# Kernel tuning notes

Hardware: AMD Instinct MI355X
Metric: run time of the kernel (lower is better)

## Reference

```python
import jax, jax.numpy as jnp
import numpy as np

EPS_RMS = 1.1920929e-07  # torch.finfo(float32).eps (nn.RMSNorm default eps=None)
EPS_LN = 1e-5
SCALE = 64 ** -0.5       # Attention.scale uses default dim_head=64, NOT dim_head_qk
SOFTCLAMP = 5.0
DEPTH = 4
H, DQK, DV = 8, 128, 192
D, DP = 768, 128
SEQ, NPAIR, B = 2048, 256, 1
FF_INNER = int(D * 2.0)
DP_INNER = int(DP * 2.0)
MAX_POS = 8192


def rmsnorm(x, w):
    return x * jax.lax.rsqrt(jnp.mean(x * x, axis=-1, keepdims=True) + EPS_RMS) * w


def layernorm_nb(x, w):  # LayerNorm(bias=False)
    mu = jnp.mean(x, axis=-1, keepdims=True)
    var = jnp.mean((x - mu) ** 2, axis=-1, keepdims=True)
    return (x - mu) * jax.lax.rsqrt(var + EPS_LN) * w


def rotate_half(x):
    x1, x2 = jnp.split(x, 2, axis=-1)
    return jnp.concatenate((-x2, x1), axis=-1)


def apply_rotary(pos, t):
    return t * jnp.cos(pos) + rotate_half(t) * jnp.sin(pos)


def rotary_table(seq_len):
    # faithful to source: inv_freq = 1/(arange(nf) + logspace(1, max_pos-nf+1, nf))
    nf = DQK // 2
    inv_freq = 1.0 / (jnp.arange(nf, dtype=jnp.float32)
                      + 10.0 ** jnp.linspace(1.0, float(MAX_POS - nf + 1), nf, dtype=jnp.float32))
    freqs = jnp.arange(seq_len, dtype=jnp.float32)[:, None] * inv_freq  # [n, nf]
    return jnp.concatenate((freqs, freqs), axis=-1)  # [n, DQK]


def softclamp(t):
    return jnp.tanh(t / SOFTCLAMP) * SOFTCLAMP


def _forward(single, pairwise, attn_pre_w, attn_post_w, qkv_w, q_norm_w, k_norm_w,
             v_norm_w, bias_rms_w, bias_proj_w, out_w, ff_pre_w, ff_post_w,
             ff_w1, ff_b1, ff_w2, ff_b2, pw_attn_pre_w, pw_qk_w, pw_v_w, pw_v_b,
             pw_ff_pre_w, pw_ff_w1, pw_ff_b1, pw_ff_w2, pw_ff_b2):
    b, n, _ = single.shape
    pos = rotary_table(n)
    pw_idx = 0
    for i in range(DEPTH):
        # ---- attention block (sandwich RMSNorm) ----
        res = single
        xn = rmsnorm(single, attn_pre_w[i])
        qkv = xn @ qkv_w[i]
        q, k, v = jnp.split(qkv, [H * DQK, H * DQK + DQK], axis=-1)
        q = q.reshape(b, n, H, DQK).transpose(0, 2, 1, 3)  # b h n d (k,v are single-head)
        q = layernorm_nb(q, q_norm_w[i]) * SCALE
        k = layernorm_nb(k, k_norm_w[i])
        v = layernorm_nb(v, v_norm_w[i])
        q = apply_rotary(pos, q)
        k = apply_rotary(pos, k)
        sim = jnp.einsum('bhid,bjd->bhij', q, k)
        # pairwise bias: RMSNorm -> GELU -> Linear(dp, heads) -> b h i j, nearest-repeat to seq
        pb = jax.nn.gelu(rmsnorm(pairwise, bias_rms_w[i]), approximate=False) @ bias_proj_w[i]
        pb = pb.transpose(0, 3, 1, 2)  # b h i j
        r = sim.shape[-1] // pb.shape[-1]
        pb = jnp.repeat(jnp.repeat(pb, r, axis=2), r, axis=3)
        attn = jax.nn.softmax(softclamp(sim + pb), axis=-1)
        out = jnp.einsum('bhij,bjd->bhid', attn, v)
        out = out.transpose(0, 2, 1, 3).reshape(b, n, H * DV)
        single = rmsnorm(out @ out_w[i], attn_post_w[i]) + res
        # ---- feedforward (sandwich RMSNorm) ----
        res = single
        xn = rmsnorm(single, ff_pre_w[i])
        h = jax.nn.relu(xn @ ff_w1[i] + ff_b1[i])
        single = rmsnorm(h @ ff_w2[i] + ff_b2[i], ff_post_w[i]) + res
        # ---- pairwise track every other layer (no sandwich) ----
        if i % 2 == 0:
            j = pw_idx
            res = pairwise
            xn = rmsnorm(pairwise, pw_attn_pre_w[j])
            pq, pk = jnp.split(xn @ pw_qk_w[j], 2, axis=-1)
            pv = xn @ pw_v_w[j] + pw_v_b[j]
            psim = jnp.einsum('bnid,bnjd->bnij', pq, pk)  # source never applies its scale
            pairwise = jnp.einsum('bnij,bnjd->bnid', jax.nn.softmax(psim, axis=-1), pv) + res
            res = pairwise
            xn = rmsnorm(pairwise, pw_ff_pre_w[j])
            hh = jax.nn.relu(xn @ pw_ff_w1[j] + pw_ff_b1[j])
            pairwise = hh @ pw_ff_w2[j] + pw_ff_b2[j] + res
            pw_idx += 1
    return single, pairwise


def setup_inputs() -> dict:
    key = jax.random.key(0)
    ks = iter(jax.random.split(key, 40))
    nrm = lambda shape: jax.random.normal(next(ks), shape, jnp.float32) * 0.02
    n_pw = (DEPTH + 1) // 2
    return dict(
        single=jax.random.normal(next(ks), (B, SEQ, D), jnp.float32),
        pairwise=jax.random.normal(next(ks), (B, NPAIR, NPAIR, DP), jnp.float32),
        attn_pre_w=jnp.ones((DEPTH, D), jnp.float32),
        attn_post_w=jnp.ones((DEPTH, D), jnp.float32),
        qkv_w=nrm((DEPTH, D, H * DQK + DQK + DV)),
        q_norm_w=jnp.ones((DEPTH, DQK), jnp.float32),
        k_norm_w=jnp.ones((DEPTH, DQK), jnp.float32),
        v_norm_w=jnp.ones((DEPTH, DV), jnp.float32),
        bias_rms_w=jnp.ones((DEPTH, DP), jnp.float32),
        bias_proj_w=nrm((DEPTH, DP, H)),
        out_w=nrm((DEPTH, H * DV, D)),
        ff_pre_w=jnp.ones((DEPTH, D), jnp.float32),
        ff_post_w=jnp.ones((DEPTH, D), jnp.float32),
        ff_w1=nrm((DEPTH, D, FF_INNER)),
        ff_b1=jnp.zeros((DEPTH, FF_INNER), jnp.float32),
        ff_w2=nrm((DEPTH, FF_INNER, D)),
        ff_b2=jnp.zeros((DEPTH, D), jnp.float32),
        pw_attn_pre_w=jnp.ones((n_pw, DP), jnp.float32),
        pw_qk_w=nrm((n_pw, DP, 2 * DP)),
        pw_v_w=nrm((n_pw, DP, DP)),
        pw_v_b=jnp.zeros((n_pw, DP), jnp.float32),
        pw_ff_pre_w=jnp.ones((n_pw, DP), jnp.float32),
        pw_ff_w1=nrm((n_pw, DP, DP_INNER)),
        pw_ff_b1=jnp.zeros((n_pw, DP_INNER), jnp.float32),
        pw_ff_w2=nrm((n_pw, DP_INNER, DP)),
        pw_ff_b2=jnp.zeros((n_pw, DP), jnp.float32),
    )


def reference(single, pairwise, attn_pre_w, attn_post_w, qkv_w, q_norm_w, k_norm_w,
              v_norm_w, bias_rms_w, bias_proj_w, out_w, ff_pre_w, ff_post_w,
              ff_w1, ff_b1, ff_w2, ff_b2, pw_attn_pre_w, pw_qk_w, pw_v_w, pw_v_b,
              pw_ff_pre_w, pw_ff_w1, pw_ff_b1, pw_ff_w2, pw_ff_b2):
    return _forward(single, pairwise, attn_pre_w, attn_post_w, qkv_w, q_norm_w,
                    k_norm_w, v_norm_w, bias_rms_w, bias_proj_w, out_w, ff_pre_w,
                    ff_post_w, ff_w1, ff_b1, ff_w2, ff_b2, pw_attn_pre_w, pw_qk_w,
                    pw_v_w, pw_v_b, pw_ff_pre_w, pw_ff_w1, pw_ff_b1, pw_ff_w2, pw_ff_b2)
```

## Files before the change

### kernel.cpp

```cpp
#include <hip/hip_runtime.h>
#include <hip/hip_bf16.h>

#define SEQ 2048
#define DMODEL 768
#define NHEAD 8
#define DQK 128
#define DV 192
#define QKVN 1344
#define FFI 1536
#define NP 256
#define DP 128
#define DPI 256
#define NPR 65536
#define KVB 64
#define NSPLIT 2

#define EPS_RMS 1.1920929e-07f
#define EPS_LN 1e-5f
#define C1_LOG2E 0.5770780163555852f
#define C2_LOG2E -14.426950408889634f

typedef __attribute__((ext_vector_type(8))) short bf16x8;
typedef __attribute__((ext_vector_type(4))) short bf16x4;
typedef __attribute__((ext_vector_type(4))) float f32x4;

__device__ inline float wave_sum(float v) {
#pragma unroll
  for (int o = 32; o > 0; o >>= 1) v += __shfl_xor(v, o, 64);
  return v;
}
__device__ inline unsigned short f2bf(float x) {
  unsigned int u = __float_as_uint(x);
  u += 0x7fffu + ((u >> 16) & 1u);
  return (unsigned short)(u >> 16);
}
__device__ inline float bf2f(unsigned short x) {
  unsigned int u = ((unsigned int)x) << 16;
  return __uint_as_float(u);
}

__global__ void pos_kernel(float* __restrict__ pos) {
  int i = blockIdx.x, l = threadIdx.x;
  float f = (l == 0) ? 0.1f * (float)i : 0.0f;
  pos[i * 128 + l] = f;
  pos[i * 128 + 64 + l] = f;
}

__global__ void rowscale_kernel(const float* __restrict__ x, float* __restrict__ sc, int cols) {
  size_t row = blockIdx.x;
  int l = threadIdx.x;
  const float* xr = x + row * cols;
  float ss = 0.f;
  for (int c = l; c < cols; c += 64) { float v = xr[c]; ss += v * v; }
  ss = wave_sum(ss);
  if (l == 0) sc[row] = rsqrtf(ss / (float)cols + EPS_RMS);
}

__global__ void rmsres_kernel(const float* __restrict__ x, const float* __restrict__ w,
                              const float* res, float* y, int cols, float* __restrict__ sc) {
  size_t row = blockIdx.x;
  int l = threadIdx.x;
  const float* xr = x + row * cols;
  float ss = 0.f;
  for (int c = l; c < cols; c += 64) { float v = xr[c]; ss += v * v; }
  ss = wave_sum(ss);
  float r = rsqrtf(ss / (float)cols + EPS_RMS);
  float* yr = y + row * cols;
  const float* rr = res + row * cols;
  float ss2 = 0.f;
  for (int c = l; c < cols; c += 64) {
    float v = xr[c] * r * w[c] + rr[c];
    yr[c] = v;
    ss2 += v * v;
  }
  ss2 = wave_sum(ss2);
  if (l == 0) sc[row] = rsqrtf(ss2 / (float)cols + EPS_RMS);
}

__global__ __launch_bounds__(256) void convT_kernel(const float* __restrict__ W,
                                                    unsigned short* __restrict__ Wt,
                                                    int K, int N) {
  __shared__ float ls[32][33];
  int n0 = blockIdx.x * 32, k0 = blockIdx.y * 32;
  int t = threadIdx.x;
  int c = t & 31, r4 = t >> 5;
#pragma unroll
  for (int p = 0; p < 4; p++) {
    int r = r4 + p * 8;
    ls[r][c] = W[(size_t)(k0 + r) * N + n0 + c];
  }
  __syncthreads();
#pragma unroll
  for (int p = 0; p < 4; p++) {
    int n = r4 + p * 8, k = t & 31;
    Wt[(size_t)(n0 + n) * K + k0 + k] = f2bf(ls[k][n]);
  }
}

__global__ void biasbuild_kernel(const float* __restrict__ pw_v_b, float* __restrict__ b384) {
  int j = blockIdx.x, t = threadIdx.x;
  b384[j * 384 + t] = (t < 256) ? 0.f : pw_v_b[j * DP + t - 256];
}

template<int ABF, int CBF, int ACMB = 0>
__global__ __launch_bounds__(256) void gemm_k(const void* __restrict__ Av,
    const unsigned short* __restrict__ Bt, void* __restrict__ Cv,
    int M, int N, int K, int nbx,
    const float* __restrict__ bias, const float* __restrict__ resid, int act,
    const float* __restrict__ ascale, const float* __restrict__ aw,
    const float* __restrict__ lb = nullptr) {
  __shared__ unsigned short As[64 * 32];
  __shared__ unsigned short Bs[128 * 32];
  int t = threadIdx.x;
  int nwg = gridDim.x, bid = blockIdx.x;
  int qq = nwg >> 3, rr = nwg & 7, xc = bid & 7, ii = bid >> 3;
  int swz = (xc < rr ? xc * (qq + 1) : rr * (qq + 1) + (xc - rr) * qq) + ii;
  int bm = (swz / nbx) * 64, bn = (swz % nbx) * 128;
  int w = t >> 6, l = t & 63;
  int wr = (w >> 1) * 32, wc = (w & 1) * 64;
  int lo = l & 15, hi = l >> 4;
  f32x4 acc[2][4];
#pragma unroll
  for (int q = 0; q < 2; q++)
#pragma unroll
    for (int cb = 0; cb < 4; cb++) acc[q][cb] = (f32x4){0.f, 0.f, 0.f, 0.f};

  int arow = t >> 2, acs = (t & 3) * 8;
  int brow = t >> 1, bks = (t & 1) * 16;
  int bok = (bn + brow < N);
  const unsigned short* bsrc = Bt + (size_t)(bok ? bn + brow : 0) * K + bks;

  float4 pa0, pa1;
  bf16x8 pab, pc1, pb0, pb1;
  float linv = 1.f;
  const bf16x8 zb = {0, 0, 0, 0, 0, 0, 0, 0};

  {
    if (ACMB) {
      const unsigned short* Op = (const unsigned short*)Av;
      size_t base = (size_t)(bm + arow) * K + acs;
      pab = *(const bf16x8*)(Op + base);
      pc1 = *(const bf16x8*)(Op + (size_t)SEQ * K + base);
      int h = acs / DV;
      linv = 1.0f / (lb[(size_t)h * SEQ + bm + arow] +
                     lb[(size_t)(NHEAD + h) * SEQ + bm + arow]);
    } else if (ABF) {
      pab = *(const bf16x8*)((const unsigned short*)Av + (size_t)(bm + arow) * K + acs);
    } else {
      const float* A = (const float*)Av;
      pa0 = *(const float4*)(A + (size_t)(bm + arow) * K + acs);
      pa1 = *(const float4*)(A + (size_t)(bm + arow) * K + acs + 4);
    }
    pb0 = bok ? *(const bf16x8*)(bsrc) : zb;
    pb1 = bok ? *(const bf16x8*)(bsrc + 8) : zb;
  }

  for (int k0 = 0; k0 < K; k0 += 32) {
    if (k0) __syncthreads();
    {
      int byte = (arow * 64 + acs * 2) ^ ((arow & 7) << 4);
      if (ACMB) {
        bf16x8 cmb;
#pragma unroll
        for (int e = 0; e < 8; e++)
          cmb[e] = (short)f2bf((bf2f((unsigned short)pab[e]) +
                                bf2f((unsigned short)pc1[e])) * linv);
        *(bf16x8*)((char*)As + byte) = cmb;
      } else if (ABF) {
        *(bf16x8*)((char*)As + byte) = pab;
      } else {
        float4 v0 = pa0, v1 = pa1;
        if (ascale) {
          float s = ascale[bm + arow];
          v0.x *= s * aw[k0 + acs + 0]; v0.y *= s * aw[k0 + acs + 1];
          v0.z *= s * aw[k0 + acs + 2]; v0.w *= s * aw[k0 + acs + 3];
          v1.x *= s * aw[k0 + acs + 4]; v1.y *= s * aw[k0 + acs + 5];
          v1.z *= s * aw[k0 + acs + 6]; v1.w *= s * aw[k0 + acs + 7];
        }
        uint4 pk;
        pk.x = (unsigned int)f2bf(v0.x) | ((unsigned int)f2bf(v0.y) << 16);
        pk.y = (unsigned int)f2bf(v0.z) | ((unsigned int)f2bf(v0.w) << 16);
        pk.z = (unsigned int)f2bf(v1.x) | ((unsigned int)f2bf(v1.y) << 16);
        pk.w = (unsigned int)f2bf(v1.z) | ((unsigned int)f2bf(v1.w) << 16);
        *(uint4*)((char*)As + byte) = pk;
      }
      int b0 = (brow * 64 + bks * 2) ^ ((brow & 7) << 4);
      int b1 = (brow * 64 + bks * 2 + 16) ^ ((brow & 7) << 4);
      *(bf16x8*)((char*)Bs + b0) = pb0;
      *(bf16x8*)((char*)Bs + b1) = pb1;
    }
    __syncthreads();
    if (k0 + 32 < K) {
      int kn = k0 + 32;
      if (ACMB) {
        const unsigned short* Op = (const unsigned short*)Av;
        size_t base = (size_t)(bm + arow) * K + kn + acs;
        pab = *(const bf16x8*)(Op + base);
        pc1 = *(const bf16x8*)(Op + (size_t)SEQ * K + base);
        int h = (kn + acs) / DV;
        linv = 1.0f / (lb[(size_t)h * SEQ + bm + arow] +
                       lb[(size_t)(NHEAD + h) * SEQ + bm + arow]);
      } else if (ABF) {
        pab = *(const bf16x8*)((const unsigned short*)Av + (size_t)(bm + arow) * K + kn + acs);
      } else {
        const float* A = (const float*)Av;
        pa0 = *(const float4*)(A + (size_t)(bm + arow) * K + kn + acs);
        pa1 = *(const float4*)(A + (size_t)(bm + arow) * K + kn + acs + 4);
      }
      pb0 = bok ? *(const bf16x8*)(bsrc + kn) : zb;
      pb1 = bok ? *(const bf16x8*)(bsrc + kn + 8) : zb;
    }
    bf16x8 af[2], bfr[4];
#pragma unroll
    for (int q = 0; q < 2; q++) {
      int r = wr + q * 16 + lo;
      af[q] = *(const bf16x8*)((char*)As + ((r * 64 + hi * 16) ^ ((r & 7) << 4)));
    }
#pragma unroll
    for (int cb = 0; cb < 4; cb++) {
      int n = wc + cb * 16 + lo;
      bfr[cb] = *(const bf16x8*)((char*)Bs + ((n * 64 + hi * 16) ^ ((n & 7) << 4)));
    }
#pragma unroll
    for (int q = 0; q < 2; q++)
#pragma unroll
      for (int cb = 0; cb < 4; cb++)
        acc[q][cb] = __builtin_amdgcn_mfma_f32_16x16x32_bf16(af[q], bfr[cb], acc[q][cb], 0, 0, 0);
  }
#pragma unroll
  for (int q = 0; q < 2; q++) {
#pragma unroll
    for (int cb = 0; cb < 4; cb++) {
      int gn = bn + wc + cb * 16 + lo;
      if (gn >= N) continue;
#pragma unroll
      for (int i = 0; i < 4; i++) {
        int gm = bm + wr + q * 16 + hi * 4 + i;
        float v = acc[q][cb][i];
        if (bias) v += bias[gn];
        if (act) v = fmaxf(v, 0.f);
        if (CBF) {
          ((unsigned short*)Cv)[(size_t)gm * N + gn] = f2bf(v);
        } else {
          if (resid) v += resid[(size_t)gm * N + gn];
          ((float*)Cv)[(size_t)gm * N + gn] = v;
        }
      }
    }
  }
}

__global__ void qkv_prep_kernel(const float* __restrict__ qkv, const float* __restrict__ qw,
                                const float* __restrict__ kw, const float* __restrict__ vw,
                                const float* __restrict__ pos,
                                unsigned short* __restrict__ q_r, unsigned short* __restrict__ k_n,
                                unsigned short* __restrict__ v_t) {
  int i = blockIdx.x;
  int y = blockIdx.y;
  int l = threadIdx.x;
  if (y == 9) {
    const float* row = qkv + (size_t)i * QKVN + NHEAD * DQK + DQK;
    float x0 = row[l], x1 = row[l + 64], x2 = row[l + 128];
    float mu = wave_sum(x0 + x1 + x2) * (1.0f / 192.0f);
    float d0 = x0 - mu, d1 = x1 - mu, d2 = x2 - mu;
    float var = wave_sum(d0 * d0 + d1 * d1 + d2 * d2) * (1.0f / 192.0f);
    float rs = rsqrtf(var + EPS_LN);
    v_t[(size_t)l * SEQ + i] = f2bf(d0 * rs * vw[l]);
    v_t[(size_t)(l + 64) * SEQ + i] = f2bf(d1 * rs * vw[l + 64]);
    v_t[(size_t)(l + 128) * SEQ + i] = f2bf(d2 * rs * vw[l + 128]);
    return;
  }
  int off = (y < 8) ? y * DQK : NHEAD * DQK;
  const float* row = qkv + (size_t)i * QKVN + off;
  float a = row[l], b = row[l + 64];
  float mu = wave_sum(a + b) * (1.0f / 128.0f);
  float da = a - mu, db = b - mu;
  float var = wave_sum(da * da + db * db) * (1.0f / 128.0f);
  float rs = rsqrtf(var + EPS_LN);
  const float* w = (y < 8) ? qw : kw;
  float na = da * rs * w[l], nb = db * rs * w[l + 64];
  if (y < 8) { na *= 0.125f; nb *= 0.125f; }
  float p0 = pos[i * 128 + l], p1 = pos[i * 128 + 64 + l];
  float ra = na * cosf(p0) - nb * sinf(p0);
  float rb = nb * cosf(p1) + na * sinf(p1);
  if (y < 8) {
    unsigned short* o = q_r + ((size_t)y * SEQ + i) * DQK;
    o[l] = f2bf(ra); o[l + 64] = f2bf(rb);
  } else {
    unsigned short* o = k_n + (size_t)i * DQK;
    o[l] = f2bf(ra); o[l + 64] = f2bf(rb);
  }
}

__global__ __launch_bounds__(256) void pb_kernel(const float* __restrict__ P,
    float* __restrict__ scP, const float* __restrict__ rmsw,
    const float* __restrict__ proj, float* __restrict__ pbt) {
  __shared__ float gs[32][130];
  __shared__ float projs[1024];
  int b = blockIdx.x, t = threadIdx.x;
  int row0 = b * 32;
  int wv = t >> 6, ln = t & 63;
  for (int f = t; f < 1024; f += 256) projs[f] = proj[f];
#pragma unroll
  for (int rr = 0; rr < 8; rr++) {
    int r = wv * 8 + rr;
    const float* src = P + (size_t)(row0 + r) * DP;
    float2 x = *(const float2*)(src + ln * 2);
    float ss = wave_sum(x.x * x.x + x.y * x.y);
    float rs = rsqrtf(ss * (1.0f / DP) + EPS_RMS);
    float g0 = x.x * rs * rmsw[ln * 2];
    float g1 = x.y * rs * rmsw[ln * 2 + 1];
    gs[r][ln * 2] = 0.5f * g0 * (1.0f + erff(g0 * 0.70710678118654752f));
    gs[r][ln * 2 + 1] = 0.5f * g1 * (1.0f + erff(g1 * 0.70710678118654752f));
    if (ln == 0) scP[row0 + r] = rs;
  }
  __syncthreads();
  int hh = t >> 5, r = t & 31;
  float acc = 0.f;
#pragma unroll 4
  for (int d = 0; d < 128; d++) acc += gs[r][d] * projs[d * 8 + hh];
  pbt[(size_t)hh * NPR + row0 + r] = acc;
}

__global__ __launch_bounds__(256) void attn_mfma(const unsigned short* __restrict__ q_r,
    const unsigned short* __restrict__ k_n, const unsigned short* __restrict__ v_t,
    const float* __restrict__ pbt, unsigned short* __restrict__ Opart,
    float* __restrict__ lbuf) {
  __shared__ unsigned short Ks[64 * 128];
  __shared__ unsigned short Vs[208 * 64];
  __shared__ unsigned short Ps[4][16 * 64];
  __shared__ float pb_lds[64];
  int ib = blockIdx.x, h = blockIdx.y, sp = blockIdx.z, t = threadIdx.x;
  int i0 = ib * 64;
  int w = t >> 6, l = t & 63;
  int lo = l & 15, hi = l >> 4;
  int kbeg = sp * (SEQ / NSPLIT), kend = kbeg + SEQ / NSPLIT;

  bf16x8 qf[4];
  {
    const unsigned short* qp = q_r + ((size_t)h * SEQ + i0 + w * 16 + lo) * DQK + hi * 8;
#pragma unroll
    for (int ks = 0; ks < 4; ks++) qf[ks] = *(const bf16x8*)(qp + ks * 32);
  }
  f32x4 o_acc[13];
#pragma unroll
  for (int vc = 0; vc < 13; vc++) o_acc[vc] = (f32x4){0.f, 0.f, 0.f, 0.f};

#pragma unroll
  for (int r4 = 0; r4 < 4; r4++) {
    int idx = t + 256 * r4;
    int row = 192 + (idx >> 6), key = idx & 63;
    int byte = (row * 128 + key * 2) ^ ((row & 7) << 4);
    *(unsigned short*)((char*)Vs + byte) = (row == 192) ? 0x3F80 : 0;
  }

  char* PsW = (char*)&Ps[w][0];
  int rg8 = (((w * 16 + lo) >> 3) << 3) + (hi >> 1);

  for (int k0 = kbeg; k0 < kend; k0 += KVB) {
    {
      int row = t >> 2, d0 = (t & 3) * 32;
      const unsigned short* src = k_n + (size_t)(k0 + row) * DQK + d0;
#pragma unroll
      for (int jj = 0; jj < 4; jj++) {
        bf16x8 a = *(const bf16x8*)(src + jj * 8);
        int byte = (row * 256 + (d0 + jj * 8) * 2) ^ ((row & 7) << 4);
        *(bf16x8*)((char*)Ks + byte) = a;
      }
    }
#pragma unroll
    for (int rep = 0; rep < 6; rep++) {
      int c = t + 256 * rep;
      int row = c >> 3, seg = c & 7;
      bf16x8 a = *(const bf16x8*)(v_t + (size_t)row * SEQ + k0 + seg * 8);
      int byte = (row * 128 + seg * 16) ^ ((row & 7) << 4);
      *(bf16x8*)((char*)Vs + byte) = a;
    }
    if (t < 64) {
      int rg = t >> 3, kg = t & 7;
      pb_lds[t] = C1_LOG2E * pbt[(size_t)h * NPR + ((i0 >> 3) + rg) * 256 + (k0 >> 3) + kg];
    }
    __syncthreads();
    f32x4 sacc[4];
#pragma unroll
    for (int kb = 0; kb < 4; kb++) sacc[kb] = (f32x4){0.f, 0.f, 0.f, 0.f};
#pragma unroll
    for (int ks = 0; ks < 4; ks++) {
#pragma unroll
      for (int kb = 0; kb < 4; kb++) {
        int key = kb * 16 + lo;
        int byte = (key * 256 + (ks * 32 + hi * 8) * 2) ^ ((key & 7) << 4);
        bf16x8 kf = *(const bf16x8*)((char*)Ks + byte);
        sacc[kb] = __builtin_amdgcn_mfma_f32_16x16x32_bf16(kf, qf[ks], sacc[kb], 0, 0, 0);
      }
    }
#pragma unroll
    for (int kb = 0; kb < 4; kb++) {
      float pb = pb_lds[rg8 + kb * 2];
      bf16x4 pk;
#pragma unroll
      for (int i = 0; i < 4; i++) {
        float x2 = fmaf(C1_LOG2E, sacc[kb][i], pb);
        float e = __builtin_amdgcn_exp2f(x2);
        float p = __builtin_amdgcn_exp2f(C2_LOG2E * __builtin_amdgcn_rcpf(e + 1.f));
        pk[i] = (short)f2bf(p);
      }
      int byte = (lo * 128 + (kb * 32 + hi * 8)) ^ ((lo & 7) << 4);
      *(bf16x4*)(PsW + byte) = pk;
    }
#pragma unroll
    for (int ks2 = 0; ks2 < 2; ks2++) {
      int byte = (lo * 128 + (ks2 * 32 + hi * 8) * 2) ^ ((lo & 7) << 4);
      bf16x8 pa = *(const bf16x8*)(PsW + byte);
#pragma unroll
      for (int vc = 0; vc < 13; vc++) {
        int dv = vc * 16 + lo;
        int vbyte = (dv * 128 + (ks2 * 32 + hi * 8) * 2) ^ ((dv & 7) << 4);
        bf16x8 bv = *(const bf16x8*)((char*)Vs + vbyte);
        o_acc[vc] = __builtin_amdgcn_mfma_f32_16x16x32_bf16(pa, bv, o_acc[vc], 0, 0, 0);
      }
    }
    __syncthreads();
  }
#pragma unroll
  for (int i = 0; i < 4; i++) {
    int row = i0 + w * 16 + hi * 4 + i;
    unsigned short* orow = Opart + (size_t)sp * SEQ * (NHEAD * DV) +
                           (size_t)row * (NHEAD * DV) + h * DV;
#pragma unroll
    for (int vc = 0; vc < 12; vc++) orow[vc * 16 + lo] = f2bf(o_acc[vc][i]);
    if (lo == 0) lbuf[((size_t)sp * NHEAD + h) * SEQ + row] = o_acc[12][i];
  }
}

__global__ __launch_bounds__(256) void pw_attn_mfma(const unsigned short* __restrict__ pqkv,
    const float* __restrict__ resid, float* __restrict__ out, int nbase,
    float* __restrict__ scP) {
  __shared__ unsigned short Ks[64 * 128];
  __shared__ unsigned short Vs[128 * 64];
  __shared__ unsigned short Ps[4][16 * 64];
  int qb = blockIdx.x, nl = blockIdx.y, t = threadIdx.x;
  int i0 = qb * 64;
  int w = t >> 6, l = t & 63;
  int lo = l & 15, hi = l >> 4;
  size_t nrow = (size_t)nl * NP;

  bf16x8 qf[4];
  {
    const unsigned short* qp = pqkv + (nrow + i0 + w * 16 + lo) * 384 + hi * 8;
#pragma unroll
    for (int ks = 0; ks < 4; ks++) qf[ks] = *(const bf16x8*)(qp + ks * 32);
  }
  float m_s[4], l_s[4];
  f32x4 o_acc[8];
#pragma unroll
  for (int i = 0; i < 4; i++) { m_s[i] = -1e30f; l_s[i] = 0.f; }
#pragma unroll
  for (int vc = 0; vc < 8; vc++) o_acc[vc] = (f32x4){0.f, 0.f, 0.f, 0.f};
  char* PsW = (char*)&Ps[w][0];

  for (int k0 = 0; k0 < NP; k0 += 64) {
    {
      int row = t >> 2, d0 = (t & 3) * 32;
      const unsigned short* src = pqkv + (nrow + k0 + row) * 384 + DP + d0;
#pragma unroll
      for (int jj = 0; jj < 4; jj++) {
        bf16x8 a = *(const bf16x8*)(src + jj * 8);
        int byte = (row * 256 + (d0 + jj * 8) * 2) ^ ((row & 7) << 4);
        *(bf16x8*)((char*)Ks + byte) = a;
      }
    }
    {
      int key = t & 63, ds0 = (t >> 6) * 32;
      const unsigned short* src = pqkv + (nrow + k0 + key) * 384 + 256 + ds0;
#pragma unroll
      for (int e = 0; e < 4; e++) {
        bf16x8 a = *(const bf16x8*)(src + e * 8);
#pragma unroll
        for (int e2 = 0; e2 < 8; e2++) {
          int dv = ds0 + e * 8 + e2;
          *(unsigned short*)((char*)Vs + ((dv * 128 + key * 2) ^ ((dv & 7) << 4))) =
              (unsigned short)a[e2];
        }
      }
    }
    __syncthreads();
    f32x4 sacc[4];
#pragma unroll
    for (int cs = 0; cs < 4; cs++) sacc[cs] = (f32x4){0.f, 0.f, 0.f, 0.f};
#pragma unroll
    for (int ks = 0; ks < 4; ks++) {
#pragma unroll
      for (int cs = 0; cs < 4; cs++) {
        int key = cs * 16 + lo;
        int byte = (key * 256 + (ks * 32 + hi * 8) * 2) ^ ((key & 7) << 4);
        bf16x8 bk = *(const bf16x8*)((char*)Ks + byte);
        sacc[cs] = __builtin_amdgcn_mfma_f32_16x16x32_bf16(qf[ks], bk, sacc[cs], 0, 0, 0);
      }
    }
#pragma unroll
    for (int i = 0; i < 4; i++) {
      float mrow = fmaxf(fmaxf(sacc[0][i], sacc[1][i]), fmaxf(sacc[2][i], sacc[3][i]));
#pragma unroll
      for (int ofs = 1; ofs < 16; ofs <<= 1) mrow = fmaxf(mrow, __shfl_xor(mrow, ofs, 64));
      float mn = fmaxf(m_s[i], mrow);
      float scale = __expf(m_s[i] - mn);
      float ts = 0.f;
      int r = hi * 4 + i;
#pragma unroll
      for (int cs = 0; cs < 4; cs++) {
        float p = __expf(sacc[cs][i] - mn);
        ts += p;
        int key = cs * 16 + lo;
        int byte = (r * 128 + key * 2) ^ ((r & 7) << 4);
        *(unsigned short*)(PsW + byte) = f2bf(p);
      }
#pragma unroll
      for (int ofs = 1; ofs < 16; ofs <<= 1) ts += __shfl_xor(ts, ofs, 64);
      l_s[i] = l_s[i] * scale + ts;
      m_s[i] = mn;
#pragma unroll
      for (int vc = 0; vc < 8; vc++) o_acc[vc][i] *= scale;
    }
#pragma unroll
    for (int ks2 = 0; ks2 < 2; ks2++) {
      int byte = (lo * 128 + (ks2 * 32 + hi * 8) * 2) ^ ((lo & 7) << 4);
      bf16x8 pa = *(const bf16x8*)(PsW + byte);
#pragma unroll
      for (int vc = 0; vc < 8; vc++) {
        int dv = vc * 16 + lo;
        int vbyte = (dv * 128 + (ks2 * 32 + hi * 8) * 2) ^ ((dv & 7) << 4);
        bf16x8 bv = *(const bf16x8*)((char*)Vs + vbyte);
        o_acc[vc] = __builtin_amdgcn_mfma_f32_16x16x32_bf16(pa, bv, o_acc[vc], 0, 0, 0);
      }
    }
    __syncthreads();
  }
#pragma unroll
  for (int i = 0; i < 4; i++) {
    float inv = 1.0f / l_s[i];
    size_t growi = (size_t)(nbase + nl) * NP + i0 + w * 16 + hi * 4 + i;
    size_t grow = growi * DP;
    float ss = 0.f;
#pragma unroll
    for (int vc = 0; vc < 8; vc++) {
      int dv = vc * 16 + lo;
      float v = o_acc[vc][i] * inv + resid[grow + dv];
      out[grow + dv] = v;
      ss += v * v;
    }
#pragma unroll
    for (int ofs = 1; ofs < 16; ofs <<= 1) ss += __shfl_xor(ss, ofs, 64);
    if (lo == 0) scP[growi] = rsqrtf(ss * (1.0f / DP) + EPS_RMS);
  }
}

extern "C" void kernel_launch(void* const* d_in, const int* in_sizes, int n_in,
                              void* d_out, int out_size, void* d_ws, size_t ws_size,
                              hipStream_t stream) {
  const float* in_single   = (const float*)d_in[0];
  const float* in_pair     = (const float*)d_in[1];
  const float* attn_pre_w  = (const float*)d_in[2];
  const float* attn_post_w = (const float*)d_in[3];
  const float* qkv_w       = (const float*)d_in[4];
  const float* q_norm_w    = (const float*)d_in[5];
  const float* k_norm_w    = (const float*)d_in[6];
  const float* v_norm_w    = (const float*)d_in[7];
  const float* bias_rms_w  = (const float*)d_in[8];
  const float* bias_proj_w = (const float*)d_in[9];
  const float* out_w       = (const float*)d_in[10];
  const float* ff_pre_w    = (const float*)d_in[11];
  const float* ff_post_w   = (const float*)d_in[12];
  const float* ff_w1       = (const float*)d_in[13];
  const float* ff_b1       = (const float*)d_in[14];
  const float* ff_w2       = (const float*)d_in[15];
  const float* ff_b2       = (const float*)d_in[16];
  const float* pw_attn_pre = (const float*)d_in[17];
  const float* pw_qk_w     = (const float*)d_in[18];
  const float* pw_v_w      = (const float*)d_in[19];
  const float* pw_v_b      = (const float*)d_in[20];
  const float* pw_ff_pre   = (const float*)d_in[21];
  const float* pw_ff_w1    = (const float*)d_in[22];
  const float* pw_ff_b1    = (const float*)d_in[23];
  const float* pw_ff_w2    = (const float*)d_in[24];
  const float* pw_ff_b2    = (const float*)d_in[25];

  float* ws = (float*)d_ws;
  float* S    = ws;
  float* Pc   = ws + 1572864;
  float* Pa   = ws + 9961472;
  float* pbt  = ws + 18350080;
  float* pos  = ws + 18874368;
  float* scP  = ws + 19136512;
  float* scS  = ws + 19202048;
  float* TMP  = ws + 19204096;
  float* qkv  = TMP;
  unsigned short* q_r_bf = (unsigned short*)(TMP + 2752512);
  unsigned short* k_n_bf = (unsigned short*)(TMP + 3801088);
  unsigned short* v_t_bf = (unsigned short*)(TMP + 3932160);
  unsigned short* WtA = (unsigned short*)(TMP + 7274496);
  unsigned short* WtX = (unsigned short*)TMP;
  float* t2   = TMP + 655360;
  unsigned short* t1_bf = (unsigned short*)(TMP + 2752512);
  unsigned short* Opart = (unsigned short*)Pa;
  float* lbuf = Pa + 6500000;
  unsigned short* WtEF = (unsigned short*)(TMP + 6300000);
  unsigned short* WtG  = (unsigned short*)(TMP + 6350000);
  unsigned short* WtH  = (unsigned short*)(TMP + 6383000);
  float* bias384       = TMP + 6420000;
  unsigned short* pqkv_bf = (unsigned short*)TMP;
  unsigned short* hh_bf   = (unsigned short*)TMP;

  float* outS = (float*)d_out;
  float* outP = outS + (size_t)SEQ * DMODEL;

  hipMemcpyAsync(S, in_single, 1572864 * sizeof(float), hipMemcpyDeviceToDevice, stream);
  hipMemcpyAsync(Pc, in_pair, (size_t)8388608 * sizeof(float), hipMemcpyDeviceToDevice, stream);
  pos_kernel<<<SEQ, 64, 0, stream>>>(pos);
  rowscale_kernel<<<SEQ, 64, 0, stream>>>(S, scS, DMODEL);
  for (int j = 0; j < 2; j++) {
    convT_kernel<<<dim3(256 / 32, DP / 32), 256, 0, stream>>>(
        pw_qk_w + (size_t)j * DP * 2 * DP, WtEF + (size_t)j * 384 * DP, DP, 2 * DP);
    convT_kernel<<<dim3(DP / 32, DP / 32), 256, 0, stream>>>(
        pw_v_w + (size_t)j * DP * DP, WtEF + (size_t)j * 384 * DP + 256 * DP, DP, DP);
    convT_kernel<<<dim3(DPI / 32, DP / 32), 256, 0, stream>>>(
        pw_ff_w1 + (size_t)j * DP * DPI, WtG + (size_t)j * DPI * DP, DP, DPI);
    convT_kernel<<<dim3(DP / 32, DPI / 32), 256, 0, stream>>>(
        pw_ff_w2 + (size_t)j * DPI * DP, WtH + (size_t)j * DP * DPI, DPI, DP);
  }
  biasbuild_kernel<<<2, 384, 0, stream>>>(pw_v_b, bias384);

  for (int i = 0; i < 4; i++) {
    int j = i / 2;
    const float* Psrc = (i == 3) ? outP : Pc;
    pb_kernel<<<2048, 256, 0, stream>>>(Psrc, scP, bias_rms_w + i * DP,
                                        bias_proj_w + (size_t)i * DP * 8, pbt);
    convT_kernel<<<dim3(QKVN / 32, DMODEL / 32), 256, 0, stream>>>(
        qkv_w + (size_t)i * DMODEL * QKVN, WtA, DMODEL, QKVN);
    gemm_k<0, 0><<<11 * 32, 256, 0, stream>>>(S, WtA, qkv, SEQ, QKVN, DMODEL, 11,
                                              nullptr, nullptr, 0, scS, attn_pre_w + i * DMODEL);
    qkv_prep_kernel<<<dim3(SEQ, 10), 64, 0, stream>>>(qkv, q_norm_w + i * DQK,
                                                      k_norm_w + i * DQK, v_norm_w + i * DV,
                                                      pos, q_r_bf, k_n_bf, v_t_bf);
    attn_mfma<<<dim3(SEQ / 64, NHEAD, NSPLIT), 256, 0, stream>>>(q_r_bf, k_n_bf, v_t_bf, pbt,
                                                                 Opart, lbuf);
    convT_kernel<<<dim3(DMODEL / 32, (NHEAD * DV) / 32), 256, 0, stream>>>(
        out_w + (size_t)i * (NHEAD * DV) * DMODEL, WtX, NHEAD * DV, DMODEL);
    gemm_k<1, 0, 1><<<6 * 32, 256, 0, stream>>>(Opart, WtX, t2, SEQ, DMODEL, NHEAD * DV, 6,
                                                nullptr, nullptr, 0, nullptr, nullptr, lbuf);
    rmsres_kernel<<<SEQ, 64, 0, stream>>>(t2, attn_post_w + i * DMODEL, S, S, DMODEL, scS);
    convT_kernel<<<dim3(FFI / 32, DMODEL / 32), 256, 0, stream>>>(
        ff_w1 + (size_t)i * DMODEL * FFI, WtX, DMODEL, FFI);
    gemm_k<0, 1><<<12 * 32, 256, 0, stream>>>(S, WtX, t1_bf, SEQ, FFI, DMODEL, 12,
                                              ff_b1 + i * FFI, nullptr, 1, scS, ff_pre_w + i * DMODEL);
    convT_kernel<<<dim3(DMODEL / 32, FFI / 32), 256, 0, stream>>>(
        ff_w2 + (size_t)i * FFI * DMODEL, WtX, FFI, DMODEL);
    gemm_k<1, 0><<<6 * 32, 256, 0, stream>>>(t1_bf, WtX, t2, SEQ, DMODEL, FFI, 6,
                                             ff_b2 + i * DMODEL, nullptr, 0, nullptr, nullptr);
    float* Sdst = (i == 3) ? outS : S;
    rmsres_kernel<<<SEQ, 64, 0, stream>>>(t2, ff_post_w + i * DMODEL, S, Sdst, DMODEL, scS);
    if ((i & 1) == 0) {
      float* Pdst = (i == 2) ? outP : Pc;
      for (int c = 0; c < 2; c++) {
        const float* Ac = Pc + (size_t)c * 32768 * DP;
        const float* sc = scP + c * 32768;
        gemm_k<0, 1><<<3 * 512, 256, 0, stream>>>(Ac, WtEF + (size_t)j * 384 * DP, pqkv_bf,
                                                  32768, 384, DP, 3,
                                                  bias384 + j * 384, nullptr, 0,
                                                  sc, pw_attn_pre + j * DP);
        pw_attn_mfma<<<dim3(4, 128), 256, 0, stream>>>(pqkv_bf, Pc, Pa, c * 128,
                                                       scP + c * 32768);
      }
      for (int c = 0; c < 2; c++) {
        const float* Ac = Pa + (size_t)c * 32768 * DP;
        const float* sc = scP + c * 32768;
        gemm_k<0, 1><<<2 * 512, 256, 0, stream>>>(Ac, WtG + (size_t)j * DPI * DP, hh_bf,
                                                  32768, DPI, DP, 2,
                                                  pw_ff_b1 + j * DPI, nullptr, 1,
                                                  sc, pw_ff_pre + j * DP);
        gemm_k<1, 0><<<1 * 512, 256, 0, stream>>>(hh_bf, WtH + (size_t)j * DP * DPI,
                                                  Pdst + (size_t)c * 32768 * DP,
                                                  32768, DP, DPI, 1,
                                                  pw_ff_b2 + j * DP, Ac, 0, nullptr, nullptr);
      }
    }
  }
}
```

Baseline: 1.288 ms.

## Split attention KV four ways, emit bf16 QKV, use exp2 softmax

Raises the attention KV split count from 2 to 4 to launch more workgroups, and widens the fused combine in the output-projection GEMM to sum four partials and four normalizers. Switches the QKV projection GEMM to write bf16 and makes the prep kernel read bf16, halving that intermediate traffic. Replaces expf in the online softmax with exp2 on log2e-prescaled values. The risks are extra partial-output memory traffic in the combine and slightly lower precision of the QKV activations.

```diff
diff --git a/kernel.cpp b/kernel.cpp
--- a/kernel.cpp
+++ b/kernel.cpp
@@ -13,10 +13,11 @@
 #define DPI 256
 #define NPR 65536
 #define KVB 64
-#define NSPLIT 2
+#define NSPLIT 4
 
 #define EPS_RMS 1.1920929e-07f
 #define EPS_LN 1e-5f
+#define LOG2E 1.4426950408889634f
 #define C1_LOG2E 0.5770780163555852f
 #define C2_LOG2E -14.426950408889634f
 
@@ -131,7 +132,7 @@
   const unsigned short* bsrc = Bt + (size_t)(bok ? bn + brow : 0) * K + bks;
 
   float4 pa0, pa1;
-  bf16x8 pab, pc1, pb0, pb1;
+  bf16x8 pab, pc1, pc2, pc3, pb0, pb1;
   float linv = 1.f;
   const bf16x8 zb = {0, 0, 0, 0, 0, 0, 0, 0};
 
@@ -141,9 +142,13 @@
       size_t base = (size_t)(bm + arow) * K + acs;
       pab = *(const bf16x8*)(Op + base);
       pc1 = *(const bf16x8*)(Op + (size_t)SEQ * K + base);
+      pc2 = *(const bf16x8*)(Op + (size_t)2 * SEQ * K + base);
+      pc3 = *(const bf16x8*)(Op + (size_t)3 * SEQ * K + base);
       int h = acs / DV;
       linv = 1.0f / (lb[(size_t)h * SEQ + bm + arow] +
-                     lb[(size_t)(NHEAD + h) * SEQ + bm + arow]);
+                     lb[(size_t)(NHEAD + h) * SEQ + bm + arow] +
+                     lb[(size_t)(2 * NHEAD + h) * SEQ + bm + arow] +
+                     lb[(size_t)(3 * NHEAD + h) * SEQ + bm + arow]);
     } else if (ABF) {
       pab = *(const bf16x8*)((const unsigned short*)Av + (size_t)(bm + arow) * K + acs);
     } else {
@@ -164,7 +169,9 @@
 #pragma unroll
         for (int e = 0; e < 8; e++)
           cmb[e] = (short)f2bf((bf2f((unsigned short)pab[e]) +
-                                bf2f((unsigned short)pc1[e])) * linv);
+                                bf2f((unsigned short)pc1[e]) +
+                                bf2f((unsigned short)pc2[e]) +
+                                bf2f((unsigned short)pc3[e])) * linv);
         *(bf16x8*)((char*)As + byte) = cmb;
       } else if (ABF) {
         *(bf16x8*)((char*)As + byte) = pab;
@@ -197,9 +204,13 @@
         size_t base = (size_t)(bm + arow) * K + kn + acs;
         pab = *(const bf16x8*)(Op + base);
         pc1 = *(const bf16x8*)(Op + (size_t)SEQ * K + base);
+        pc2 = *(const bf16x8*)(Op + (size_t)2 * SEQ * K + base);
+        pc3 = *(const bf16x8*)(Op + (size_t)3 * SEQ * K + base);
         int h = (kn + acs) / DV;
         linv = 1.0f / (lb[(size_t)h * SEQ + bm + arow] +
-                       lb[(size_t)(NHEAD + h) * SEQ + bm + arow]);
+                       lb[(size_t)(NHEAD + h) * SEQ + bm + arow] +
+                       lb[(size_t)(2 * NHEAD + h) * SEQ + bm + arow] +
+                       lb[(size_t)(3 * NHEAD + h) * SEQ + bm + arow]);
       } else if (ABF) {
         pab = *(const bf16x8*)((const unsigned short*)Av + (size_t)(bm + arow) * K + kn + acs);
       } else {
@@ -250,7 +261,8 @@
   }
 }
 
-__global__ void qkv_prep_kernel(const float* __restrict__ qkv, const float* __restrict__ qw,
+__global__ void qkv_prep_kernel(const unsigned short* __restrict__ qkv,
+                                const float* __restrict__ qw,
                                 const float* __restrict__ kw, const float* __restrict__ vw,
                                 const float* __restrict__ pos,
                                 unsigned short* __restrict__ q_r, unsigned short* __restrict__ k_n,
@@ -259,8 +271,8 @@
   int y = blockIdx.y;
   int l = threadIdx.x;
   if (y == 9) {
-    const float* row = qkv + (size_t)i * QKVN + NHEAD * DQK + DQK;
-    float x0 = row[l], x1 = row[l + 64], x2 = row[l + 128];
+    const unsigned short* row = qkv + (size_t)i * QKVN + NHEAD * DQK + DQK;
+    float x0 = bf2f(row[l]), x1 = bf2f(row[l + 64]), x2 = bf2f(row[l + 128]);
     float mu = wave_sum(x0 + x1 + x2) * (1.0f / 192.0f);
     float d0 = x0 - mu, d1 = x1 - mu, d2 = x2 - mu;
     float var = wave_sum(d0 * d0 + d1 * d1 + d2 * d2) * (1.0f / 192.0f);
@@ -271,8 +283,8 @@
     return;
   }
   int off = (y < 8) ? y * DQK : NHEAD * DQK;
-  const float* row = qkv + (size_t)i * QKVN + off;
-  float a = row[l], b = row[l + 64];
+  const unsigned short* row = qkv + (size_t)i * QKVN + off;
+  float a = bf2f(row[l]), b = bf2f(row[l + 64]);
   float mu = wave_sum(a + b) * (1.0f / 128.0f);
   float da = a - mu, db = b - mu;
   float var = wave_sum(da * da + db * db) * (1.0f / 128.0f);
@@ -504,12 +516,13 @@
 #pragma unroll
       for (int ofs = 1; ofs < 16; ofs <<= 1) mrow = fmaxf(mrow, __shfl_xor(mrow, ofs, 64));
       float mn = fmaxf(m_s[i], mrow);
-      float scale = __expf(m_s[i] - mn);
+      float mnl = mn * LOG2E;
+      float scale = __builtin_amdgcn_exp2f(fmaf(m_s[i], LOG2E, -mnl));
       float ts = 0.f;
       int r = hi * 4 + i;
 #pragma unroll
       for (int cs = 0; cs < 4; cs++) {
-        float p = __expf(sacc[cs][i] - mn);
+        float p = __builtin_amdgcn_exp2f(fmaf(sacc[cs][i], LOG2E, -mnl));
         ts += p;
         int key = cs * 16 + lo;
         int byte = (r * 128 + key * 2) ^ ((r & 7) << 4);
@@ -594,7 +607,7 @@
   float* scP  = ws + 19136512;
   float* scS  = ws + 19202048;
   float* TMP  = ws + 19204096;
-  float* qkv  = TMP;
+  unsigned short* qkv_bf = (unsigned short*)TMP;
   unsigned short* q_r_bf = (unsigned short*)(TMP + 2752512);
   unsigned short* k_n_bf = (unsigned short*)(TMP + 3801088);
   unsigned short* v_t_bf = (unsigned short*)(TMP + 3932160);
@@ -637,9 +650,9 @@
                                         bias_proj_w + (size_t)i * DP * 8, pbt);
     convT_kernel<<<dim3(QKVN / 32, DMODEL / 32), 256, 0, stream>>>(
         qkv_w + (size_t)i * DMODEL * QKVN, WtA, DMODEL, QKVN);
-    gemm_k<0, 0><<<11 * 32, 256, 0, stream>>>(S, WtA, qkv, SEQ, QKVN, DMODEL, 11,
+    gemm_k<0, 1><<<11 * 32, 256, 0, stream>>>(S, WtA, qkv_bf, SEQ, QKVN, DMODEL, 11,
                                               nullptr, nullptr, 0, scS, attn_pre_w + i * DMODEL);
-    qkv_prep_kernel<<<dim3(SEQ, 10), 64, 0, stream>>>(qkv, q_norm_w + i * DQK,
+    qkv_prep_kernel<<<dim3(SEQ, 10), 64, 0, stream>>>(qkv_bf, q_norm_w + i * DQK,
                                                       k_norm_w + i * DQK, v_norm_w + i * DV,
                                                       pos, q_r_bf, k_n_bf, v_t_bf);
     attn_mfma<<<dim3(SEQ / 64, NHEAD, NSPLIT), 256, 0, stream>>>(q_r_bf, k_n_bf, v_t_bf, pbt,
```

Measured after the change: 1.334 ms. 3.6% more time.
